# Performance work log

Measured on AMD Instinct MI355X. Metric: run time of the kernel, lower is better.

The kernel has to match this reference:

```python
import jax, jax.numpy as jnp
import numpy as np

B, T, D = 1, 2048, 4096
H, KV, HD = 32, 8, 128
R = 128           # virtual kv tokens
N_REP = H // KV   # GQA repeat factor
MAX_ALPHA = 0.5
INIT_ALPHA = 0.1
EPS = 1e-6
NEG = -1e9


def rms_norm(x, w):
    # Qwen3 RMSNorm over last dim (head_dim)
    var = jnp.mean(jnp.square(x), axis=-1, keepdims=True)
    return x * jax.lax.rsqrt(var + EPS) * w


def rotate_half(x):
    x1, x2 = jnp.split(x, 2, axis=-1)
    return jnp.concatenate([-x2, x1], axis=-1)


def setup_inputs() -> dict:
    key = jax.random.key(0)
    ks = jax.random.split(key, 8)
    hidden_states = jax.random.normal(ks[0], (B, T, D), dtype=jnp.float32)
    # additive causal mask [B,1,T,T]: 0 on/below diag, -1e9 above
    causal = jnp.where(jnp.arange(T)[:, None] >= jnp.arange(T)[None, :], 0.0, NEG)
    attention_mask = jnp.broadcast_to(causal, (B, 1, T, T)).astype(jnp.float32)
    # RoPE tables [T, HD]
    inv_freq = 1.0 / (10000.0 ** (np.arange(0, HD, 2, dtype=np.float32) / HD))
    angles = np.arange(T, dtype=np.float32)[:, None] * inv_freq[None, :]
    emb = np.concatenate([angles, angles], axis=-1)
    cos = jnp.asarray(np.cos(emb), dtype=jnp.float32)
    sin = jnp.asarray(np.sin(emb), dtype=jnp.float32)
    virtual_keys = jax.random.normal(ks[1], (B, KV, R, HD), dtype=jnp.float32)
    virtual_values = jax.random.normal(ks[2], (B, KV, R, HD), dtype=jnp.float32)
    s = 1.0 / np.sqrt(D)
    Wq = jax.random.normal(ks[3], (D, H * HD), dtype=jnp.float32) * s
    Wk = jax.random.normal(ks[4], (D, KV * HD), dtype=jnp.float32) * s
    Wv = jax.random.normal(ks[5], (D, KV * HD), dtype=jnp.float32) * s
    Wo = jax.random.normal(ks[6], (H * HD, D), dtype=jnp.float32) * s
    q_norm_w = jnp.ones((HD,), dtype=jnp.float32)
    k_norm_w = jnp.ones((HD,), dtype=jnp.float32)
    init_logit = float(np.log(INIT_ALPHA / (MAX_ALPHA - INIT_ALPHA + 1e-8)))
    alpha_logit = jnp.asarray(init_logit, dtype=jnp.float32)
    return {
        "hidden_states": hidden_states, "attention_mask": attention_mask,
        "cos": cos, "sin": sin,
        "virtual_keys": virtual_keys, "virtual_values": virtual_values,
        "Wq": Wq, "Wk": Wk, "Wv": Wv, "Wo": Wo,
        "q_norm_w": q_norm_w, "k_norm_w": k_norm_w,
        "alpha_logit": alpha_logit,
    }


def reference(hidden_states, attention_mask, cos, sin, virtual_keys,
              virtual_values, Wq, Wk, Wv, Wo, q_norm_w, k_norm_w, alpha_logit):
    b, t, _ = hidden_states.shape
    # projections -> [B, heads, T, HD]
    q = rms_norm((hidden_states @ Wq).reshape(b, t, H, HD), q_norm_w).transpose(0, 2, 1, 3)
    k = rms_norm((hidden_states @ Wk).reshape(b, t, KV, HD), k_norm_w).transpose(0, 2, 1, 3)
    v = (hidden_states @ Wv).reshape(b, t, KV, HD).transpose(0, 2, 1, 3)
    # RoPE
    c = cos[None, None]; s = sin[None, None]
    q = q * c + rotate_half(q) * s
    k = k * c + rotate_half(k) * s
    # virtual KV injection, alpha = max_alpha * sigmoid(logit) * inference_scale(=1)
    alpha = MAX_ALPHA * jax.nn.sigmoid(alpha_logit)
    k = jnp.concatenate([virtual_keys * alpha, k], axis=2)
    v = jnp.concatenate([virtual_values * alpha, v], axis=2)
    vmask = jnp.zeros((b, 1, t, R), dtype=attention_mask.dtype)
    mask = jnp.concatenate([vmask, attention_mask], axis=-1)  # [B,1,T,R+T]
    # repeat_kv for GQA
    k = jnp.repeat(k, N_REP, axis=1)
    v = jnp.repeat(v, N_REP, axis=1)
    scaling = HD ** -0.5
    scores = jnp.einsum('bhqd,bhkd->bhqk', q, k) * scaling + mask
    w = jax.nn.softmax(scores.astype(jnp.float32), axis=-1).astype(q.dtype)
    out = jnp.einsum('bhqk,bhkd->bhqd', w, v)           # [B,H,T,HD]
    out = out.transpose(0, 2, 1, 3).reshape(b, t, H * HD)
    return out @ Wo


if __name__ == '__main__':
    o = reference(**setup_inputs())
    print(o.shape, o.dtype)
```

## Files before the change

kernel.cpp:

```cpp
#include <hip/hip_runtime.h>
#include <hip/hip_bf16.h>

#define T_SEQ 2048
#define DMODEL 4096
#define NH 32
#define NKV 8
#define HD 128
#define RVIRT 128
#define TKV (RVIRT + T_SEQ)

typedef __attribute__((ext_vector_type(8))) short s16x8;
typedef __attribute__((ext_vector_type(4))) short s16x4;
typedef __attribute__((ext_vector_type(4))) float f32x4;
typedef __attribute__((ext_vector_type(4))) float float4v;

static __device__ __forceinline__ short f2bf(float f) {
  union { __hip_bfloat16 h; short s; } u; u.h = __float2bfloat16(f); return u.s;
}

static __device__ __forceinline__ void gload16(const void* g, void* l) {
  __builtin_amdgcn_global_load_lds(
      (const __attribute__((address_space(1))) void*)g,
      (__attribute__((address_space(3))) void*)l, 16, 0, 0);
}

#define TOPSYNC() \
  __builtin_amdgcn_s_barrier(); \
  asm volatile("s_waitcnt lgkmcnt(0)" ::: "memory"); \
  __builtin_amdgcn_sched_barrier(0);

__global__ __launch_bounds__(256) void convert_x(const float* __restrict__ src,
                                                 short* __restrict__ dst)
{
  int i = (blockIdx.x * 256 + threadIdx.x) * 8;
  float4v a = *(const float4v*)(src + i);
  float4v b = *(const float4v*)(src + i + 4);
  s16x8 o;
#pragma unroll
  for (int j = 0; j < 4; ++j) { o[j] = f2bf(a[j]); o[4 + j] = f2bf(b[j]); }
  *(s16x8*)(dst + i) = o;
}

__global__ __launch_bounds__(256) void transpose_convert(const float* __restrict__ src,
    short* __restrict__ dst, int K, int N)
{
  __shared__ float tile[64][65];
  const int k0 = blockIdx.y * 64, n0 = blockIdx.x * 64;
  const int tid = threadIdx.x;
  const int rr = tid >> 4, c4 = (tid & 15) * 4;
#pragma unroll
  for (int it = 0; it < 4; ++it) {
    int row = it * 16 + rr;
    float4v v = *(const float4v*)(src + (size_t)(k0 + row) * N + n0 + c4);
    tile[row][c4] = v[0]; tile[row][c4 + 1] = v[1];
    tile[row][c4 + 2] = v[2]; tile[row][c4 + 3] = v[3];
  }
  __syncthreads();
  const int n = tid >> 3, seg = tid & 7;
#pragma unroll
  for (int it = 0; it < 2; ++it) {
    int nn = it * 32 + n;
    s16x8 o;
#pragma unroll
    for (int j = 0; j < 8; ++j) o[j] = f2bf(tile[seg * 8 + j][nn]);
    *(s16x8*)(dst + (size_t)(n0 + nn) * K + k0 + seg * 8) = o;
  }
}

__global__ __launch_bounds__(512, 2) void gemm_qkv(const short* __restrict__ Ab,
    const short* __restrict__ Btb, float* __restrict__ C0,
    float* __restrict__ Ck, short* __restrict__ Cv, int K)
{
  constexpr int SLOT = 57344;
  __shared__ __align__(16) char lds[2 * SLOT];
  const int tid = threadIdx.x, lane = tid & 63, w = tid >> 6;
  const int lo = lane & 15, g = lane >> 4;
  const int wm = w >> 1, wn = w & 1;
  const int m0 = blockIdx.y * 256, n0 = blockIdx.x * 192;
  const int NT = K >> 6;
  const int aswz = (lo & 7) << 4;
  const int t8 = tid >> 3, t7 = tid & 7;
  const int swc = (t7 ^ (t8 & 7)) * 8;

  const short* As = Ab + (size_t)(m0 + t8) * K + swc;
  const short* Bs[3];
#pragma unroll
  for (int jj = 0; jj < 3; ++jj) {
    int row = (t8 >> 5) * 96 + (2 * jj + ((t8 >> 4) & 1)) * 16 + (t8 & 15);
    Bs[jj] = Btb + (size_t)(n0 + row) * K + swc;
  }
  auto SA = [&](char* nb, int jj, int y) {
    gload16(As + (size_t)jj * 64 * K + y * 64, nb + tid * 16 + jj * 8192);
  };
  auto SB = [&](char* nb, int jj, int y) {
    gload16(Bs[jj] + y * 64, nb + 32768 + tid * 16 + jj * 8192);
  };

  f32x4 acc[4][6];
#pragma unroll
  for (int i = 0; i < 4; ++i)
#pragma unroll
    for (int j = 0; j < 6; ++j) acc[i][j] = (f32x4){0.f, 0.f, 0.f, 0.f};

  s16x8 a[4][2], bq[2][2];

#define QLDB(P) \
  _Pragma("unroll") for (int jj = 0; jj < 2; ++jj) \
  _Pragma("unroll") for (int kk = 0; kk < 2; ++kk) \
    bq[jj][kk] = *(const s16x8*)(bu + 32768 + ((P) * 64 + wn * 32 + jj * 16 + lo) * 128 + ((kk * 64 + g * 16) ^ aswz));
#define QMMQ(P) \
  __builtin_amdgcn_s_setprio(1); \
  _Pragma("unroll") for (int i = 0; i < 4; ++i) \
  _Pragma("unroll") for (int jj = 0; jj < 2; ++jj) { \
    f32x4 z = __builtin_amdgcn_mfma_f32_16x16x32_bf16(a[i][0], bq[jj][0], acc[i][(P) * 2 + jj], 0, 0, 0); \
    acc[i][(P) * 2 + jj] = __builtin_amdgcn_mfma_f32_16x16x32_bf16(a[i][1], bq[jj][1], z, 0, 0, 0); \
  } \
  __builtin_amdgcn_s_setprio(0);

  SA(lds, 0, 0); SA(lds, 1, 0); SA(lds, 2, 0); SA(lds, 3, 0);
  SB(lds, 0, 0); SB(lds, 1, 0); SB(lds, 2, 0);
  asm volatile("s_waitcnt vmcnt(0)" ::: "memory");
  __builtin_amdgcn_s_barrier();

  for (int t = 0; t < NT; ++t) {
    const char* bu = lds + (t & 1) * SLOT;
    char* nb = lds + ((t + 1) & 1) * SLOT;
    const bool pre = (t + 1 < NT);
#pragma unroll
    for (int i = 0; i < 4; ++i)
#pragma unroll
      for (int kk = 0; kk < 2; ++kk)
        a[i][kk] = *(const s16x8*)(bu + (wm * 64 + i * 16 + lo) * 128 + ((kk * 64 + g * 16) ^ aswz));
    QLDB(0);
    if (pre) { SA(nb, 0, t + 1); SA(nb, 1, t + 1); SA(nb, 2, t + 1); }
    TOPSYNC();
    QMMQ(0);
    if (pre) asm volatile("s_waitcnt vmcnt(4)" ::: "memory");
    else     asm volatile("s_waitcnt vmcnt(1)" ::: "memory");
    __builtin_amdgcn_s_barrier();
    QLDB(1);
    if (pre) { SA(nb, 3, t + 1); SB(nb, 0, t + 1); }
    TOPSYNC();
    QMMQ(1);
    if (pre) asm volatile("s_waitcnt vmcnt(5)" ::: "memory");
    else     asm volatile("s_waitcnt vmcnt(0)" ::: "memory");
    __builtin_amdgcn_s_barrier();
    QLDB(2);
    if (pre) { SB(nb, 1, t + 1); SB(nb, 2, t + 1); }
    TOPSYNC();
    QMMQ(2);
    if (pre) asm volatile("s_waitcnt vmcnt(2)" ::: "memory");
    __builtin_amdgcn_s_barrier();
  }
#undef QLDB
#undef QMMQ

#pragma unroll
  for (int i = 0; i < 4; ++i)
#pragma unroll
    for (int j = 0; j < 6; ++j)
#pragma unroll
      for (int r = 0; r < 4; ++r) {
        int row = m0 + wm * 64 + i * 16 + g * 4 + r;
        int col = n0 + wn * 96 + j * 16 + lo;
        float val = acc[i][j][r];
        if (col < 4096) C0[(size_t)row * 4096 + col] = val;
        else if (col < 5120) Ck[(size_t)row * 1024 + (col - 4096)] = val;
        else {
          int vcol = col - 5120;
          int d = vcol & 127;
          int rp = (RVIRT + row) ^ ((((d >> 3) ^ d) & 7) << 3);
          Cv[((size_t)(vcol >> 7) * HD + d) * TKV + rp] = f2bf(val);
        }
      }
}

__global__ __launch_bounds__(512, 2) void gemm_out(const short* __restrict__ Ab,
    const short* __restrict__ Btb, float* __restrict__ C0, int K)
{
  constexpr int SLOT = 49152;
  __shared__ __align__(16) char lds[2 * SLOT];
  const int tid = threadIdx.x, lane = tid & 63, w = tid >> 6;
  const int lo = lane & 15, g = lane >> 4;
  const int wm = w >> 2, wn = w & 3;
  const int m0 = blockIdx.y * 128, n0 = blockIdx.x * 256;
  const int NT = K >> 6;
  const int aswz = (lo & 7) << 4;
  const int t8 = tid >> 3, t7 = tid & 7;
  const int swc = (t7 ^ (t8 & 7)) * 8;

  const short* As = Ab + (size_t)(m0 + t8) * K + swc;
  const short* Bs[4];
#pragma unroll
  for (int jj = 0; jj < 4; ++jj) {
    int row = (t8 >> 4) * 64 + jj * 16 + (t8 & 15);
    Bs[jj] = Btb + (size_t)(n0 + row) * K + swc;
  }
  auto SA = [&](char* nb, int jj, int y) {
    gload16(As + (size_t)jj * 64 * K + y * 64, nb + tid * 16 + jj * 8192);
  };
  auto SB = [&](char* nb, int jj, int y) {
    gload16(Bs[jj] + y * 64, nb + 16384 + tid * 16 + jj * 8192);
  };

  f32x4 acc[4][4];
#pragma unroll
  for (int i = 0; i < 4; ++i)
#pragma unroll
    for (int j = 0; j < 4; ++j) acc[i][j] = (f32x4){0.f, 0.f, 0.f, 0.f};

  s16x8 a[4][2], bq[2][2];

#define OLDB(P) \
  _Pragma("unroll") for (int jj = 0; jj < 2; ++jj) \
  _Pragma("unroll") for (int kk = 0; kk < 2; ++kk) \
    bq[jj][kk] = *(const s16x8*)(bu + 16384 + (((P) * 2 + jj) * 64 + wn * 16 + lo) * 128 + ((kk * 64 + g * 16) ^ aswz));
#define OMMQ(P) \
  __builtin_amdgcn_s_setprio(1); \
  _Pragma("unroll") for (int i = 0; i < 4; ++i) \
  _Pragma("unroll") for (int jj = 0; jj < 2; ++jj) { \
    f32x4 z = __builtin_amdgcn_mfma_f32_16x16x32_bf16(a[i][0], bq[jj][0], acc[i][(P) * 2 + jj], 0, 0, 0); \
    acc[i][(P) * 2 + jj] = __builtin_amdgcn_mfma_f32_16x16x32_bf16(a[i][1], bq[jj][1], z, 0, 0, 0); \
  } \
  __builtin_amdgcn_s_setprio(0);

  SA(lds, 0, 0); SA(lds, 1, 0);
  SB(lds, 0, 0); SB(lds, 1, 0); SB(lds, 2, 0); SB(lds, 3, 0);
  asm volatile("s_waitcnt vmcnt(0)" ::: "memory");
  __builtin_amdgcn_s_barrier();

  for (int t = 0; t < NT; ++t) {
    const char* bu = lds + (t & 1) * SLOT;
    char* nb = lds + ((t + 1) & 1) * SLOT;
    const bool pre = (t + 1 < NT);
#pragma unroll
    for (int i = 0; i < 4; ++i)
#pragma unroll
      for (int kk = 0; kk < 2; ++kk)
        a[i][kk] = *(const s16x8*)(bu + (wm * 64 + i * 16 + lo) * 128 + ((kk * 64 + g * 16) ^ aswz));
    OLDB(0);
    if (pre) { SA(nb, 0, t + 1); SA(nb, 1, t + 1); SB(nb, 0, t + 1); SB(nb, 1, t + 1); }
    TOPSYNC();
    OMMQ(0);
    if (pre) asm volatile("s_waitcnt vmcnt(4)" ::: "memory");
    else     asm volatile("s_waitcnt vmcnt(0)" ::: "memory");
    __builtin_amdgcn_s_barrier();
    OLDB(1);
    if (pre) { SB(nb, 2, t + 1); SB(nb, 3, t + 1); }
    TOPSYNC();
    OMMQ(1);
    if (pre) asm volatile("s_waitcnt vmcnt(2)" ::: "memory");
    __builtin_amdgcn_s_barrier();
  }
#undef OLDB
#undef OMMQ

#pragma unroll
  for (int i = 0; i < 4; ++i)
#pragma unroll
    for (int j = 0; j < 4; ++j)
#pragma unroll
      for (int r = 0; r < 4; ++r) {
        int row = m0 + wm * 64 + i * 16 + g * 4 + r;
        int col = n0 + wn * 64 + j * 16 + lo;
        C0[(size_t)row * 4096 + col] = acc[i][j][r];
      }
}

__global__ __launch_bounds__(256) void rope_kernel(const float* __restrict__ proj,
    const float* __restrict__ nw, const float* __restrict__ cosT,
    const float* __restrict__ sinT, short* __restrict__ out,
    int nh_shift, int rows_total, int row0, float qs, int kswz)
{
  int wid = blockIdx.x * 4 + (threadIdx.x >> 6);
  int lane = threadIdx.x & 63;
  int nh = 1 << nh_shift;
  int t = wid >> nh_shift;
  int hh = wid & (nh - 1);
  const float* src = proj + (size_t)t * (nh * HD) + hh * HD;
  float x1 = src[lane];
  float x2 = src[lane + 64];
  float ss = x1 * x1 + x2 * x2;
#pragma unroll
  for (int off = 32; off > 0; off >>= 1) ss += __shfl_xor(ss, off, 64);
  float rms = rsqrtf(ss * (1.0f / 128.0f) + 1e-6f);
  float n1 = x1 * rms * nw[lane];
  float n2 = x2 * rms * nw[lane + 64];
  float c1 = cosT[t * HD + lane], c2 = cosT[t * HD + lane + 64];
  float s1 = sinT[t * HD + lane], s2 = sinT[t * HD + lane + 64];
  short* dst = out + ((size_t)hh * rows_total + row0 + t) * HD;
  int sw = kswz ? (((row0 + t) & 7) << 3) : 0;
  dst[lane ^ sw]        = f2bf((n1 * c1 - n2 * s1) * qs);
  dst[(lane + 64) ^ sw] = f2bf((n2 * c2 + n1 * s2) * qs);
}

__global__ __launch_bounds__(256) void inject_kernel(const float* __restrict__ vk,
    const float* __restrict__ vv, const float* __restrict__ logit,
    short* __restrict__ Kr, short* __restrict__ Vt)
{
  int idx = blockIdx.x * 256 + threadIdx.x;
  float alpha = 0.5f / (1.0f + __expf(-logit[0]));
  int kv = idx >> 14, rem = idx & 16383, r = rem >> 7, d = rem & 127;
  int swk = (r & 7) << 3;
  Kr[((size_t)kv * TKV + r) * HD + (d ^ swk)] = f2bf(vk[idx] * alpha);
  int swv = ((d ^ (d >> 3)) & 7) << 3;
  Vt[((size_t)kv * HD + d) * TKV + (r ^ swv)] = f2bf(vv[idx] * alpha);
}

__global__ __launch_bounds__(256, 2) void attn_kernel(const short* __restrict__ Qr,
    const short* __restrict__ Kr, const short* __restrict__ Vt,
    short* __restrict__ out)
{
  __shared__ short Ks[2][64 * 128];
  __shared__ short Vs[2][128 * 64];
  __shared__ __align__(16) char Ps[4 * 4096];
  const int tid = threadIdx.x, lane = tid & 63, w = tid >> 6;
  const int bid = blockIdx.x;
  const int kvh = bid & 7;
  const int r5 = bid >> 3;
  const int h = kvh * 4 + (r5 & 3);
  const int bx = r5 >> 2;
  const int lo = lane & 15, g = lane >> 4;
  const int q0A = bx * 64, q0B = (31 - bx) * 64;
  const int ntA = bx + 3, ntB = 34 - bx;
  char* PsA = Ps + w * 4096;
  char* PsB = PsA + 2048;
  const short* Kb = Kr + (size_t)kvh * TKV * HD;
  const short* Vb = Vt + (size_t)kvh * HD * TKV;

  s16x8 qfA[4], qfB[4];
#pragma unroll
  for (int kk = 0; kk < 4; ++kk) {
    qfA[kk] = *(const s16x8*)(Qr + ((size_t)h * T_SEQ + q0A + w * 16 + lo) * HD + kk * 32 + g * 8);
    qfB[kk] = *(const s16x8*)(Qr + ((size_t)h * T_SEQ + q0B + w * 16 + lo) * HD + kk * 32 + g * 8);
  }
  const int qrA = q0A + w * 16 + lo, qrB = q0B + w * 16 + lo;

  float mA = -3.0e38f, lA = 0.f, mB = -3.0e38f, lB = 0.f;
  f32x4 oA[8] = {}, oB[8] = {};

  auto STAGE = [&](int kvt, int buf) {
#pragma unroll
    for (int p = 0; p < 4; ++p) {
      int ci = p * 256 + tid;
      gload16(Kb + (size_t)(kvt * 64 + (ci >> 4)) * HD + (ci & 15) * 8,
              (char*)Ks[buf] + ci * 16);
      gload16(Vb + (size_t)(ci >> 3) * TKV + kvt * 64 + (ci & 7) * 8,
              (char*)Vs[buf] + ci * 16);
    }
  };

  STAGE(0, 0);
  asm volatile("s_waitcnt vmcnt(0)" ::: "memory");
  __syncthreads();

  for (int kvt = 0; kvt < ntB; ++kvt) {
    const int cur = kvt & 1;
    if (kvt + 1 < ntB) STAGE(kvt + 1, cur ^ 1);
    const char* Ksb = (const char*)Ks[cur];
    const char* Vsb = (const char*)Vs[cur];
    const bool doA = (kvt < ntA);
    const bool maskA = (kvt == ntA - 1);
    const bool maskB = (kvt == ntB - 1);

    f32x4 sA[4], sB[4];
    __builtin_amdgcn_s_setprio(1);
#pragma unroll
    for (int cj = 0; cj < 4; ++cj) {
      f32x4 zA = {}, zB = {};
      const int kr = cj * 16 + lo;
#pragma unroll
      for (int kk = 0; kk < 4; ++kk) {
        s16x8 kf = *(const s16x8*)(Ksb + ((kr * 256 + kk * 64 + g * 16) ^ ((kr & 7) << 4)));
        zB = __builtin_amdgcn_mfma_f32_16x16x32_bf16(kf, qfB[kk], zB, 0, 0, 0);
        if (doA) zA = __builtin_amdgcn_mfma_f32_16x16x32_bf16(kf, qfA[kk], zA, 0, 0, 0);
      }
      sA[cj] = zA; sB[cj] = zB;
    }
    __builtin_amdgcn_s_setprio(0);

#define SOFTMAX(S, M, L, O, PSW, MASKED, QR) { \
      float mx = -3.0e38f; \
      _Pragma("unroll") for (int cj = 0; cj < 4; ++cj) \
      _Pragma("unroll") for (int r = 0; r < 4; ++r) { \
        float s = S[cj][r]; \
        if (MASKED) { \
          int k = kvt * 64 + cj * 16 + g * 4 + r; \
          bool ok = (k < RVIRT) || (k - RVIRT <= (QR)); \
          s = ok ? s : -3.0e38f; S[cj][r] = s; \
        } \
        mx = fmaxf(mx, s); \
      } \
      mx = fmaxf(mx, __shfl_xor(mx, 16, 64)); \
      mx = fmaxf(mx, __shfl_xor(mx, 32, 64)); \
      if (__any(mx > M + 8.0f)) { \
        float mnew = fmaxf(M, mx); \
        float fs = __expf(M - mnew); \
        M = mnew; L *= fs; \
        _Pragma("unroll") for (int r = 0; r < 4; ++r) { \
          float fsq = __shfl(fs, g * 4 + r, 64); \
          _Pragma("unroll") for (int dj = 0; dj < 8; ++dj) O[dj][r] *= fsq; \
        } \
      } \
      float rowsum = 0.f; \
      _Pragma("unroll") for (int cj = 0; cj < 4; ++cj) { \
        s16x4 pk; \
        _Pragma("unroll") for (int r = 0; r < 4; ++r) { \
          float pv = __expf(S[cj][r] - M); \
          rowsum += pv; pk[r] = f2bf(pv); \
        } \
        *(s16x4*)(PSW + ((lo * 128 + cj * 32 + g * 8) ^ ((lo & 7) << 4))) = pk; \
      } \
      rowsum += __shfl_xor(rowsum, 16, 64); \
      rowsum += __shfl_xor(rowsum, 32, 64); \
      L += rowsum; \
    }
    if (doA) SOFTMAX(sA, mA, lA, oA, PsA, maskA, qrA);
    SOFTMAX(sB, mB, lB, oB, PsB, maskB, qrB);
#undef SOFTMAX

    s16x8 pfA[2], pfB[2];
#pragma unroll
    for (int k2 = 0; k2 < 2; ++k2) {
      pfB[k2] = *(const s16x8*)(PsB + ((lo * 128 + k2 * 64 + g * 16) ^ ((lo & 7) << 4)));
      if (doA) pfA[k2] = *(const s16x8*)(PsA + ((lo * 128 + k2 * 64 + g * 16) ^ ((lo & 7) << 4)));
    }
    __builtin_amdgcn_s_setprio(1);
#pragma unroll
    for (int dj = 0; dj < 8; ++dj) {
      const int d = dj * 16 + lo;
      const int vswz = ((d ^ (d >> 3)) & 7) << 4;
#pragma unroll
      for (int k2 = 0; k2 < 2; ++k2) {
        s16x8 vf = *(const s16x8*)(Vsb + ((d * 128 + k2 * 64 + g * 16) ^ vswz));
        oB[dj] = __builtin_amdgcn_mfma_f32_16x16x32_bf16(pfB[k2], vf, oB[dj], 0, 0, 0);
        if (doA) oA[dj] = __builtin_amdgcn_mfma_f32_16x16x32_bf16(pfA[k2], vf, oA[dj], 0, 0, 0);
      }
    }
    __builtin_amdgcn_s_setprio(0);

    asm volatile("s_waitcnt vmcnt(0)" ::: "memory");
    __syncthreads();
  }

#pragma unroll
  for (int r = 0; r < 4; ++r) {
    float lqA = __shfl(lA, g * 4 + r, 64);
    float lqB = __shfl(lB, g * 4 + r, 64);
    float iA = 1.f / lqA, iB = 1.f / lqB;
#pragma unroll
    for (int dj = 0; dj < 8; ++dj) {
      int col = h * HD + dj * 16 + lo;
      int rowA = q0A + w * 16 + g * 4 + r;
      int rowB = q0B + w * 16 + g * 4 + r;
      out[(size_t)rowA * (NH * HD) + col] = f2bf(oA[dj][r] * iA);
      out[(size_t)rowB * (NH * HD) + col] = f2bf(oB[dj][r] * iB);
    }
  }
}

extern "C" void kernel_launch(void* const* d_in, const int* in_sizes, int n_in,
                              void* d_out, int out_size, void* d_ws, size_t ws_size,
                              hipStream_t stream)
{
  const float* hidden = (const float*)d_in[0];
  const float* cosT = (const float*)d_in[2];
  const float* sinT = (const float*)d_in[3];
  const float* vk   = (const float*)d_in[4];
  const float* vv   = (const float*)d_in[5];
  const float* Wq   = (const float*)d_in[6];
  const float* Wk   = (const float*)d_in[7];
  const float* Wv   = (const float*)d_in[8];
  const float* Wo   = (const float*)d_in[9];
  const float* qnw  = (const float*)d_in[10];
  const float* knw  = (const float*)d_in[11];
  const float* alog = (const float*)d_in[12];

  char* ws = (char*)d_ws;
  float* q_projf = (float*)ws;
  float* k_projf = (float*)(ws + 33554432);
  short* Vt      = (short*)(ws + 41943040);
  short* Qr      = (short*)(ws + 46399488);
  short* Kr      = (short*)(ws + 63176704);
  short* Xb      = (short*)(ws + 67633152);
  short* Wall    = (short*)(ws + 84410368);
  short* Wot     = Wall;
  short* attn_out = (short*)ws;
  float* outp = (float*)d_out;

  const float qscale = 0.08838834764831845f;

  dim3 blk(256);
  convert_x<<<dim3(T_SEQ * DMODEL / 8 / 256), blk, 0, stream>>>(hidden, Xb);
  transpose_convert<<<dim3(64, 64), blk, 0, stream>>>(Wq, Wall, DMODEL, 4096);
  transpose_convert<<<dim3(16, 64), blk, 0, stream>>>(Wk, Wall + (size_t)4096 * DMODEL, DMODEL, 1024);
  transpose_convert<<<dim3(16, 64), blk, 0, stream>>>(Wv, Wall + (size_t)5120 * DMODEL, DMODEL, 1024);
  gemm_qkv<<<dim3(32, 8), dim3(512), 0, stream>>>(Xb, Wall, q_projf, k_projf, Vt, DMODEL);
  rope_kernel<<<dim3(T_SEQ * NH / 4),  blk, 0, stream>>>(q_projf, qnw, cosT, sinT, Qr, 5, T_SEQ, 0, qscale, 0);
  rope_kernel<<<dim3(T_SEQ * NKV / 4), blk, 0, stream>>>(k_projf, knw, cosT, sinT, Kr, 3, TKV, RVIRT, 1.0f, 1);
  inject_kernel<<<dim3(NKV * RVIRT * HD / 256), blk, 0, stream>>>(vk, vv, alog, Kr, Vt);
  attn_kernel<<<dim3(512), blk, 0, stream>>>(Qr, Kr, Vt, attn_out);
  transpose_convert<<<dim3(64, 64), blk, 0, stream>>>(Wo, Wot, 4096, 4096);
  gemm_out<<<dim3(16, 16), dim3(512), 0, stream>>>(attn_out, Wot, outp, 4096);
}
```

Baseline: 345.2 us.

## Merge prep, rope/inject, and Wo transpose into attention launches

```diff
diff --git a/kernel.cpp b/kernel.cpp
--- a/kernel.cpp
+++ b/kernel.cpp
@@ -29,24 +29,35 @@
   asm volatile("s_waitcnt lgkmcnt(0)" ::: "memory"); \
   __builtin_amdgcn_sched_barrier(0);
 
-__global__ __launch_bounds__(256) void convert_x(const float* __restrict__ src,
-                                                 short* __restrict__ dst)
+__global__ __launch_bounds__(256) void prep_kernel(const float* __restrict__ hidden,
+    short* __restrict__ Xb, const float* __restrict__ Wq,
+    const float* __restrict__ Wk, const float* __restrict__ Wv,
+    short* __restrict__ Wall)
 {
-  int i = (blockIdx.x * 256 + threadIdx.x) * 8;
-  float4v a = *(const float4v*)(src + i);
-  float4v b = *(const float4v*)(src + i + 4);
-  s16x8 o;
-#pragma unroll
-  for (int j = 0; j < 4; ++j) { o[j] = f2bf(a[j]); o[4 + j] = f2bf(b[j]); }
-  *(s16x8*)(dst + i) = o;
-}
-
-__global__ __launch_bounds__(256) void transpose_convert(const float* __restrict__ src,
-    short* __restrict__ dst, int K, int N)
-{
+  const int bid = blockIdx.x, tid = threadIdx.x;
+  if (bid < 4096) {
+    int i = (bid * 256 + tid) * 8;
+    float4v a = *(const float4v*)(hidden + i);
+    float4v b = *(const float4v*)(hidden + i + 4);
+    s16x8 o;
+#pragma unroll
+    for (int j = 0; j < 4; ++j) { o[j] = f2bf(a[j]); o[4 + j] = f2bf(b[j]); }
+    *(s16x8*)(Xb + i) = o;
+    return;
+  }
   __shared__ float tile[64][65];
-  const int k0 = blockIdx.y * 64, n0 = blockIdx.x * 64;
-  const int tid = threadIdx.x;
+  const float* src; short* dst; int N, k0, n0;
+  if (bid < 8192) {
+    int b = bid - 4096; src = Wq; dst = Wall; N = 4096;
+    n0 = (b & 63) * 64; k0 = (b >> 6) * 64;
+  } else if (bid < 9216) {
+    int b = bid - 8192; src = Wk; dst = Wall + (size_t)4096 * DMODEL; N = 1024;
+    n0 = (b & 15) * 64; k0 = (b >> 4) * 64;
+  } else {
+    int b = bid - 9216; src = Wv; dst = Wall + (size_t)5120 * DMODEL; N = 1024;
+    n0 = (b & 15) * 64; k0 = (b >> 4) * 64;
+  }
+  const int K = DMODEL;
   const int rr = tid >> 4, c4 = (tid & 15) * 4;
 #pragma unroll
   for (int it = 0; it < 4; ++it) {
@@ -267,55 +278,97 @@
       }
 }
 
-__global__ __launch_bounds__(256) void rope_kernel(const float* __restrict__ proj,
-    const float* __restrict__ nw, const float* __restrict__ cosT,
-    const float* __restrict__ sinT, short* __restrict__ out,
-    int nh_shift, int rows_total, int row0, float qs, int kswz)
+__global__ __launch_bounds__(256) void ropeinj_kernel(
+    const float* __restrict__ q_projf, const float* __restrict__ k_projf,
+    const float* __restrict__ qnw, const float* __restrict__ knw,
+    const float* __restrict__ cosT, const float* __restrict__ sinT,
+    const float* __restrict__ vk, const float* __restrict__ vv,
+    const float* __restrict__ logit,
+    short* __restrict__ Qr, short* __restrict__ Kr, short* __restrict__ Vt,
+    float qscale)
 {
-  int wid = blockIdx.x * 4 + (threadIdx.x >> 6);
-  int lane = threadIdx.x & 63;
-  int nh = 1 << nh_shift;
-  int t = wid >> nh_shift;
-  int hh = wid & (nh - 1);
-  const float* src = proj + (size_t)t * (nh * HD) + hh * HD;
-  float x1 = src[lane];
-  float x2 = src[lane + 64];
-  float ss = x1 * x1 + x2 * x2;
-#pragma unroll
-  for (int off = 32; off > 0; off >>= 1) ss += __shfl_xor(ss, off, 64);
-  float rms = rsqrtf(ss * (1.0f / 128.0f) + 1e-6f);
-  float n1 = x1 * rms * nw[lane];
-  float n2 = x2 * rms * nw[lane + 64];
-  float c1 = cosT[t * HD + lane], c2 = cosT[t * HD + lane + 64];
-  float s1 = sinT[t * HD + lane], s2 = sinT[t * HD + lane + 64];
-  short* dst = out + ((size_t)hh * rows_total + row0 + t) * HD;
-  int sw = kswz ? (((row0 + t) & 7) << 3) : 0;
-  dst[lane ^ sw]        = f2bf((n1 * c1 - n2 * s1) * qs);
-  dst[(lane + 64) ^ sw] = f2bf((n2 * c2 + n1 * s2) * qs);
-}
-
-__global__ __launch_bounds__(256) void inject_kernel(const float* __restrict__ vk,
-    const float* __restrict__ vv, const float* __restrict__ logit,
-    short* __restrict__ Kr, short* __restrict__ Vt)
+  const int bid = blockIdx.x, tid = threadIdx.x;
+  if (bid < 20480) {
+    const float* proj; const float* nw; short* outp;
+    int nh_shift, rows_total, row0, kswz; float qs; int wid;
+    if (bid < 16384) {
+      proj = q_projf; nw = qnw; outp = Qr; nh_shift = 5;
+      rows_total = T_SEQ; row0 = 0; qs = qscale; kswz = 0;
+      wid = bid * 4 + (tid >> 6);
+    } else {
+      proj = k_projf; nw = knw; outp = Kr; nh_shift = 3;
+      rows_total = TKV; row0 = RVIRT; qs = 1.0f; kswz = 1;
+      wid = (bid - 16384) * 4 + (tid >> 6);
+    }
+    int lane = tid & 63;
+    int nh = 1 << nh_shift;
+    int t = wid >> nh_shift;
+    int hh = wid & (nh - 1);
+    const float* src = proj + (size_t)t * (nh * HD) + hh * HD;
+    float x1 = src[lane];
+    float x2 = src[lane + 64];
+    float ss = x1 * x1 + x2 * x2;
+#pragma unroll
+    for (int off = 32; off > 0; off >>= 1) ss += __shfl_xor(ss, off, 64);
+    float rms = rsqrtf(ss * (1.0f / 128.0f) + 1e-6f);
+    float n1 = x1 * rms * nw[lane];
+    float n2 = x2 * rms * nw[lane + 64];
+    float c1 = cosT[t * HD + lane], c2 = cosT[t * HD + lane + 64];
+    float s1 = sinT[t * HD + lane], s2 = sinT[t * HD + lane + 64];
+    short* dst = outp + ((size_t)hh * rows_total + row0 + t) * HD;
+    int sw = kswz ? (((row0 + t) & 7) << 3) : 0;
+    dst[lane ^ sw]        = f2bf((n1 * c1 - n2 * s1) * qs);
+    dst[(lane + 64) ^ sw] = f2bf((n2 * c2 + n1 * s2) * qs);
+  } else {
+    int idx = (bid - 20480) * 256 + tid;
+    float alpha = 0.5f / (1.0f + __expf(-logit[0]));
+    int kv = idx >> 14, rem = idx & 16383, r = rem >> 7, d = rem & 127;
+    int swk = (r & 7) << 3;
+    Kr[((size_t)kv * TKV + r) * HD + (d ^ swk)] = f2bf(vk[idx] * alpha);
+    int swv = ((d ^ (d >> 3)) & 7) << 3;
+    Vt[((size_t)kv * HD + d) * TKV + (r ^ swv)] = f2bf(vv[idx] * alpha);
+  }
+}
+
+__global__ __launch_bounds__(256, 2) void attn_wo_kernel(const short* __restrict__ Qr,
+    const short* __restrict__ Kr, const short* __restrict__ Vt,
+    short* __restrict__ out, const float* __restrict__ Wo,
+    short* __restrict__ Wot)
 {
-  int idx = blockIdx.x * 256 + threadIdx.x;
-  float alpha = 0.5f / (1.0f + __expf(-logit[0]));
-  int kv = idx >> 14, rem = idx & 16383, r = rem >> 7, d = rem & 127;
-  int swk = (r & 7) << 3;
-  Kr[((size_t)kv * TKV + r) * HD + (d ^ swk)] = f2bf(vk[idx] * alpha);
-  int swv = ((d ^ (d >> 3)) & 7) << 3;
-  Vt[((size_t)kv * HD + d) * TKV + (r ^ swv)] = f2bf(vv[idx] * alpha);
-}
-
-__global__ __launch_bounds__(256, 2) void attn_kernel(const short* __restrict__ Qr,
-    const short* __restrict__ Kr, const short* __restrict__ Vt,
-    short* __restrict__ out)
-{
-  __shared__ short Ks[2][64 * 128];
-  __shared__ short Vs[2][128 * 64];
-  __shared__ __align__(16) char Ps[4 * 4096];
-  const int tid = threadIdx.x, lane = tid & 63, w = tid >> 6;
+  __shared__ __align__(16) char smem[81920];
+  const int tid = threadIdx.x;
   const int bid = blockIdx.x;
+
+  if (bid >= 512) {
+    float* tile = (float*)smem;
+    int b = bid - 512;
+    const int n0 = (b & 63) * 64, k0 = (b >> 6) * 64;
+    const int N = 4096, K = 4096;
+    const int rr = tid >> 4, c4 = (tid & 15) * 4;
+#pragma unroll
+    for (int it = 0; it < 4; ++it) {
+      int row = it * 16 + rr;
+      float4v v = *(const float4v*)(Wo + (size_t)(k0 + row) * N + n0 + c4);
+      tile[row * 65 + c4] = v[0]; tile[row * 65 + c4 + 1] = v[1];
+      tile[row * 65 + c4 + 2] = v[2]; tile[row * 65 + c4 + 3] = v[3];
+    }
+    __syncthreads();
+    const int n = tid >> 3, seg = tid & 7;
+#pragma unroll
+    for (int it = 0; it < 2; ++it) {
+      int nn = it * 32 + n;
+      s16x8 o;
+#pragma unroll
+      for (int j = 0; j < 8; ++j) o[j] = f2bf(tile[(seg * 8 + j) * 65 + nn]);
+      *(s16x8*)(Wot + (size_t)(n0 + nn) * K + k0 + seg * 8) = o;
+    }
+    return;
+  }
+
+  short* Ks0 = (short*)smem;
+  short* Vs0 = (short*)(smem + 32768);
+  char*  Ps  = smem + 65536;
+  const int lane = tid & 63, w = tid >> 6;
   const int kvh = bid & 7;
   const int r5 = bid >> 3;
   const int h = kvh * 4 + (r5 & 3);
@@ -344,9 +397,9 @@
     for (int p = 0; p < 4; ++p) {
       int ci = p * 256 + tid;
       gload16(Kb + (size_t)(kvt * 64 + (ci >> 4)) * HD + (ci & 15) * 8,
-              (char*)Ks[buf] + ci * 16);
+              (char*)(Ks0 + buf * 8192) + ci * 16);
       gload16(Vb + (size_t)(ci >> 3) * TKV + kvt * 64 + (ci & 7) * 8,
-              (char*)Vs[buf] + ci * 16);
+              (char*)(Vs0 + buf * 8192) + ci * 16);
     }
   };
 
@@ -357,8 +410,8 @@
   for (int kvt = 0; kvt < ntB; ++kvt) {
     const int cur = kvt & 1;
     if (kvt + 1 < ntB) STAGE(kvt + 1, cur ^ 1);
-    const char* Ksb = (const char*)Ks[cur];
-    const char* Vsb = (const char*)Vs[cur];
+    const char* Ksb = (const char*)(Ks0 + cur * 8192);
+    const char* Vsb = (const char*)(Vs0 + cur * 8192);
     const bool doA = (kvt < ntA);
     const bool maskA = (kvt == ntA - 1);
     const bool maskB = (kvt == ntB - 1);
@@ -491,15 +544,10 @@
   const float qscale = 0.08838834764831845f;
 
   dim3 blk(256);
-  convert_x<<<dim3(T_SEQ * DMODEL / 8 / 256), blk, 0, stream>>>(hidden, Xb);
-  transpose_convert<<<dim3(64, 64), blk, 0, stream>>>(Wq, Wall, DMODEL, 4096);
-  transpose_convert<<<dim3(16, 64), blk, 0, stream>>>(Wk, Wall + (size_t)4096 * DMODEL, DMODEL, 1024);
-  transpose_convert<<<dim3(16, 64), blk, 0, stream>>>(Wv, Wall + (size_t)5120 * DMODEL, DMODEL, 1024);
+  prep_kernel<<<dim3(10240), blk, 0, stream>>>(hidden, Xb, Wq, Wk, Wv, Wall);
   gemm_qkv<<<dim3(32, 8), dim3(512), 0, stream>>>(Xb, Wall, q_projf, k_projf, Vt, DMODEL);
-  rope_kernel<<<dim3(T_SEQ * NH / 4),  blk, 0, stream>>>(q_projf, qnw, cosT, sinT, Qr, 5, T_SEQ, 0, qscale, 0);
-  rope_kernel<<<dim3(T_SEQ * NKV / 4), blk, 0, stream>>>(k_projf, knw, cosT, sinT, Kr, 3, TKV, RVIRT, 1.0f, 1);
-  inject_kernel<<<dim3(NKV * RVIRT * HD / 256), blk, 0, stream>>>(vk, vv, alog, Kr, Vt);
-  attn_kernel<<<dim3(512), blk, 0, stream>>>(Qr, Kr, Vt, attn_out);
-  transpose_convert<<<dim3(64, 64), blk, 0, stream>>>(Wo, Wot, 4096, 4096);
+  ropeinj_kernel<<<dim3(20992), blk, 0, stream>>>(q_projf, k_projf, qnw, knw,
+      cosT, sinT, vk, vv, alog, Qr, Kr, Vt, qscale);
+  attn_wo_kernel<<<dim3(4608), blk, 0, stream>>>(Qr, Kr, Vt, attn_out, Wo, Wot);
   gemm_out<<<dim3(16, 16), dim3(512), 0, stream>>>(attn_out, Wot, outp, 4096);
 }
```

New measurement: 314.4 us (median of 2 runs). 1.1x faster.
